# Optimization experiments

Hardware: AMD Instinct MI355X
Metric: run time of the kernel (lower is better)

The kernel has to match this reference:

```python
import jax, jax.numpy as jnp
import numpy as np

EPS = 1e-6


def _l2norm_last(x):
    return jnp.linalg.norm(x, axis=-1, keepdims=True)


def rotate_to(src, tgt):
    # rotation trick (vector-quantize-pytorch): Householder-style rotation of src onto tgt direction
    # src, tgt: (b, t, d)
    ns = _l2norm_last(src)
    nt = _l2norm_last(tgt)
    u = src / jnp.maximum(ns, EPS)
    q = tgt / jnp.maximum(nt, EPS)
    w = u + q
    w = jax.lax.stop_gradient(w / jnp.maximum(_l2norm_last(w), EPS))
    e = src
    rotated = (e
               - 2.0 * jnp.sum(e * w, axis=-1, keepdims=True) * w
               + 2.0 * jnp.sum(e * jax.lax.stop_gradient(u), axis=-1, keepdims=True) * q)
    return rotated * jax.lax.stop_gradient(nt / jnp.maximum(ns, EPS))


def _simvq_stage(res, V_i, g_i, b_i, cb_i, commit_w):
    # res: (b, t, D); V_i: (D, cd); g_i, b_i: (D,); cb_i: (cs, cd)
    # weight_norm Conv1d(k=1): W = g * V / ||V||_row
    Wn = g_i[:, None] * V_i / jnp.maximum(jnp.linalg.norm(V_i, axis=1, keepdims=True), 1e-12)
    implicit = cb_i @ Wn.T + b_i  # (cs, D) implicit codebook
    # nearest code via squared-distance argmin (cdist argmin equivalent, no_grad)
    d2 = (jnp.sum(res * res, axis=-1, keepdims=True)
          - 2.0 * jnp.einsum('btd,cd->btc', res, implicit)
          + jnp.sum(implicit * implicit, axis=-1))
    idx = jnp.argmin(d2, axis=-1)  # (b, t) int
    z_q = implicit[idx]  # gather: (b, t, D)
    commit = (jnp.mean((jax.lax.stop_gradient(res) - z_q) ** 2)
              + 0.25 * jnp.mean((res - jax.lax.stop_gradient(z_q)) ** 2))
    z_q = rotate_to(res, z_q)
    return z_q, idx, commit * commit_w


def setup_inputs() -> dict:
    key = jax.random.key(0)
    ks = jax.random.split(key, 5)
    B, D, T = 16, 512, 2048
    N, CS, CD = 9, 1024, 8
    z = jax.random.normal(ks[0], (B, D, T), dtype=jnp.float32)
    V = jax.random.normal(ks[1], (N, D, CD), dtype=jnp.float32)
    g = jax.random.uniform(ks[2], (N, D), dtype=jnp.float32, minval=0.5, maxval=1.5)
    b = jax.random.normal(ks[3], (N, D), dtype=jnp.float32) * 0.01
    CB = jax.random.normal(ks[4], (N, CS, CD), dtype=jnp.float32) * (CD ** -0.5)
    return {"z": z, "V": V, "g": g, "b": b, "CB": CB}


def reference(z, V, g, b, CB):
    # eval-mode ResidualSimVQ forward, all n_codebooks stages
    n_codebooks = V.shape[0]
    res = jnp.transpose(z, (0, 2, 1))  # (b, t, D)
    z_q = jnp.zeros_like(res)
    commitment_loss = jnp.float32(0.0)
    codes = []
    for i in range(n_codebooks):
        z_q_i, idx_i, commit_i = _simvq_stage(res, V[i], g[i], b[i], CB[i], 1.0)
        z_q = z_q + z_q_i
        res = res - z_q_i
        commitment_loss = commitment_loss + commit_i
        codes.append(idx_i)
    z_q = jnp.transpose(z_q, (0, 2, 1))  # (b, D, t)
    codes = jnp.stack(codes, axis=1)  # (b, n_codebooks, t)
    return z_q, codes, commitment_loss
```

## Files before the change

### kernel.cpp

```cpp
#include <hip/hip_runtime.h>


#define NB  16
#define DD  512
#define TT  2048
#define NCB 9
#define CS  1024
#define CD  8
#define KK  9
#define NBLK (NB * (TT / 16))
#define STGF (KK * DD * 4)
#define GAPTHR 0.015f

#define WS_WN_OFF  16384
#define WS_WNF_OFF (WS_WN_OFF  + (size_t)NCB*DD*KK*8)
#define WS_Q_OFF   (WS_WNF_OFF + (size_t)NCB*DD*KK*4)
#define WS_QF_OFF  (WS_Q_OFF   + (size_t)NCB*CS*8)

__device__ __forceinline__ void ld_lds16(const void* g, void* l) {
  __builtin_amdgcn_global_load_lds(
      (const __attribute__((address_space(1))) void*)g,
      (__attribute__((address_space(3))) void*)l, 16, 0, 0);
}

__global__ void k_wn(const float* __restrict__ V, const float* __restrict__ g,
                     const float* __restrict__ bp, double* __restrict__ wn,
                     float* __restrict__ wnf) {
  int gid = blockIdx.x * 256 + threadIdx.x;
  if (gid >= NCB * DD) return;
  int i = gid / DD, d = gid % DD;
  const float* vp = V + (size_t)gid * CD;
  double v[CD], s = 0.0;
#pragma unroll
  for (int k = 0; k < CD; k++) { v[k] = (double)vp[k]; s = fma(v[k], v[k], s); }
  double den = fmax(sqrt(s), 1e-12);
  double gg = (double)g[gid];
  double* row = wn + ((size_t)i * DD + d) * KK;
  float* fb = wnf + (size_t)i * KK * DD;
#pragma unroll
  for (int k = 0; k < CD; k++) {
    double wv = gg * v[k] / den;
    row[k] = wv;
    fb[(size_t)k * DD + d] = (float)wv;
  }
  row[CD] = (double)bp[gid];
  fb[(size_t)CD * DD + d] = bp[gid];
}

__global__ void k_q(const float* __restrict__ CBp, const float* __restrict__ bp,
                    const double* __restrict__ wn,
                    double* __restrict__ q, float* __restrict__ qf) {
  int wid = blockIdx.x * 4 + (threadIdx.x >> 6);
  int lane = threadIdx.x & 63;
  int i = wid / CS, c = wid % CS;
  const float* cb = CBp + (size_t)(i * CS + c) * CD;
  double cbv[CD];
#pragma unroll
  for (int k = 0; k < CD; k++) cbv[k] = (double)cb[k];
  const double* wnp = wn + (size_t)i * DD * KK;
  const float* bb = bp + (size_t)i * DD;
  double acc = 0.0;
#pragma unroll
  for (int j = 0; j < 8; j++) {
    int d = j * 64 + lane;
    double imp = (double)bb[d];
#pragma unroll
    for (int k = 0; k < CD; k++) imp = fma(cbv[k], wnp[(size_t)d * KK + k], imp);
    acc = fma(imp, imp, acc);
  }
#pragma unroll
  for (int o = 32; o; o >>= 1) acc += __shfl_xor(acc, o, 64);
  if (lane == 0) { q[wid] = acc; qf[wid] = (float)(0.5 * acc); }
}

__launch_bounds__(256, 2)
__global__ void k_main(const float* __restrict__ z, const float* __restrict__ CBp,
                       const double* __restrict__ wn, const float* __restrict__ wnf,
                       const double* __restrict__ qtab, const float* __restrict__ qftab,
                       float* __restrict__ out_zq, float* __restrict__ out_codes,
                       double* __restrict__ partials) {
  __shared__ __align__(16) float wbuf[2][KK * DD];
  __shared__ double cbuf[4];
  float* tile = (float*)wbuf;

  const int tid = threadIdx.x, lane = tid & 63, w = tid >> 6;
  const int bb = blockIdx.x >> 7, tg = blockIdx.x & 127;
  const int t0 = tg * 16;
  const float* zb = z + (size_t)bb * DD * TT + t0;
  const char* wfb = (const char*)wnf;

#pragma unroll
  for (int m = 0; m < 8; m++) {
    int F = tid + m * 256, d = F >> 2, qq = F & 3;
    const float4 v = *(const float4*)(zb + (size_t)d * TT + qq * 4);
    tile[d * 17 + qq * 4 + 0] = v.x; tile[d * 17 + qq * 4 + 1] = v.y;
    tile[d * 17 + qq * 4 + 2] = v.z; tile[d * 17 + qq * 4 + 3] = v.w;
  }
  __syncthreads();

  double res[4][8], ns2[4];
#pragma unroll
  for (int r = 0; r < 4; r++) {
    double s = 0.0;
#pragma unroll
    for (int j = 0; j < 8; j++) {
      res[r][j] = (double)tile[(j * 64 + lane) * 17 + (w * 4 + r)];
      s = fma(res[r][j], res[r][j], s);
    }
    ns2[r] = s;
  }
#pragma unroll
  for (int o = 32; o; o >>= 1)
#pragma unroll
    for (int r = 0; r < 4; r++) ns2[r] += __shfl_xor(ns2[r], o, 64);
  __syncthreads();

#pragma unroll
  for (int m = 0; m < 4; m++)
    ld_lds16(wfb + (w + m * 4) * 1024 + lane * 16,
             (char*)wbuf[0] + (w + m * 4) * 1024);
  if (w < 2)
    ld_lds16(wfb + (w + 16) * 1024 + lane * 16,
             (char*)wbuf[0] + (w + 16) * 1024);
  __syncthreads();

  double commit = 0.0;

  for (int i = 0; i < NCB; i++) {
    const float* wcur = wbuf[i & 1];
    if (i < NCB - 1) {
      const char* src = wfb + (size_t)(i + 1) * STGF;
      char* dst = (char*)wbuf[(i + 1) & 1];
#pragma unroll
      for (int m = 0; m < 4; m++)
        ld_lds16(src + (w + m * 4) * 1024 + lane * 16, dst + (w + m * 4) * 1024);
      if (w < 2)
        ld_lds16(src + (w + 16) * 1024 + lane * 16, dst + (w + 16) * 1024);
    }

    const float* cbbase = CBp + (size_t)i * CS * CD;
    const float* qfb = qftab + i * CS;
    const double* qb = qtab + i * CS;

    float pf[4][KK];
#pragma unroll
    for (int r = 0; r < 4; r++)
#pragma unroll
      for (int k = 0; k < KK; k++) pf[r][k] = 0.0f;
#pragma unroll
    for (int j = 0; j < 8; j++) {
      int d = j * 64 + lane;
      float wv[KK];
#pragma unroll
      for (int k = 0; k < KK; k++) wv[k] = wcur[k * DD + d];
      float rv[4];
#pragma unroll
      for (int r = 0; r < 4; r++) rv[r] = -(float)res[r][j];
#pragma unroll
      for (int r = 0; r < 4; r++)
#pragma unroll
        for (int k = 0; k < KK; k++) pf[r][k] = fmaf(rv[r], wv[k], pf[r][k]);
    }
#pragma unroll
    for (int o = 32; o; o >>= 1)
#pragma unroll
      for (int r = 0; r < 4; r++)
#pragma unroll
        for (int k = 0; k < KK; k++) pf[r][k] += __shfl_xor(pf[r][k], o, 64);

    float s1a[4], s2a[4], s1b[4], s2b[4];
    int   c1a[4], c1b[4];
#pragma unroll
    for (int r = 0; r < 4; r++) {
      s1a[r] = s2a[r] = s1b[r] = s2b[r] = 3.4e38f;
      c1a[r] = c1b[r] = 0;
    }
#pragma unroll 4
    for (int m = 0; m < 16; m += 2) {
#pragma unroll
      for (int h = 0; h < 2; h++) {
        int c = (m + h) * 64 + lane;
        const float4 c0 = *(const float4*)(cbbase + (size_t)c * CD);
        const float4 cx = *(const float4*)(cbbase + (size_t)c * CD + 4);
        float qv = qfb[c];
#pragma unroll
        for (int r = 0; r < 4; r++) {
          float s = qv;
          s = fmaf(c0.x, pf[r][0], s); s = fmaf(c0.y, pf[r][1], s);
          s = fmaf(c0.z, pf[r][2], s); s = fmaf(c0.w, pf[r][3], s);
          s = fmaf(cx.x, pf[r][4], s); s = fmaf(cx.y, pf[r][5], s);
          s = fmaf(cx.z, pf[r][6], s); s = fmaf(cx.w, pf[r][7], s);
          if (h == 0) {
            if (s < s1a[r]) { s2a[r] = s1a[r]; s1a[r] = s; c1a[r] = c; }
            else            { s2a[r] = fminf(s2a[r], s); }
          } else {
            if (s < s1b[r]) { s2b[r] = s1b[r]; s1b[r] = s; c1b[r] = c; }
            else            { s2b[r] = fminf(s2b[r], s); }
          }
        }
      }
    }
    float s1[4], s2[4]; int c1[4];
#pragma unroll
    for (int r = 0; r < 4; r++) {
      if (s1a[r] < s1b[r] || (s1a[r] == s1b[r] && c1a[r] < c1b[r])) {
        s1[r] = s1a[r]; c1[r] = c1a[r]; s2[r] = fminf(s2a[r], s1b[r]);
      } else {
        s1[r] = s1b[r]; c1[r] = c1b[r]; s2[r] = fminf(s2b[r], s1a[r]);
      }
    }
#pragma unroll
    for (int o = 32; o; o >>= 1) {
#pragma unroll
      for (int r = 0; r < 4; r++) {
        float os1 = __shfl_xor(s1[r], o, 64);
        int   oc1 = __shfl_xor(c1[r], o, 64);
        float os2 = __shfl_xor(s2[r], o, 64);
        float hi = fmaxf(s1[r], os1);
        s2[r] = fminf(fminf(s2[r], os2), hi);
        if (os1 < s1[r] || (os1 == s1[r] && oc1 < c1[r])) { s1[r] = os1; c1[r] = oc1; }
      }
    }

    double Ap[4], Cm[4];
    float cbf[4][8];
#pragma unroll
    for (int r = 0; r < 4; r++) {
      if (s2[r] - s1[r] < GAPTHR) {
        double pd[KK];
#pragma unroll
        for (int k = 0; k < KK; k++) pd[k] = 0.0;
#pragma unroll
        for (int j = 0; j < 8; j++) {
          const double* wrow = wn + ((size_t)i * DD + j * 64 + lane) * KK;
          double rv = res[r][j];
#pragma unroll
          for (int k = 0; k < KK; k++) pd[k] = fma(rv, wrow[k], pd[k]);
        }
#pragma unroll
        for (int o = 32; o; o >>= 1)
#pragma unroll
          for (int k = 0; k < KK; k++) pd[k] += __shfl_xor(pd[k], o, 64);
        double pm2[8];
#pragma unroll
        for (int k = 0; k < 8; k++) pm2[k] = -2.0 * pd[k];
        double bs = 1e300; int bc = 0;
#pragma unroll 4
        for (int m = 0; m < 16; m++) {
          int c = m * 64 + lane;
          const float* cb2 = cbbase + (size_t)c * CD;
          double s = qb[c];
#pragma unroll
          for (int k = 0; k < 8; k++) s = fma((double)cb2[k], pm2[k], s);
          if (s < bs) { bs = s; bc = c; }
        }
#pragma unroll
        for (int o = 32; o; o >>= 1) {
          double obs = __shfl_xor(bs, o, 64);
          int    obc = __shfl_xor(bc, o, 64);
          if (obs < bs || (obs == bs && obc < bc)) { bs = obs; bc = obc; }
        }
        c1[r] = bc;
      }
      int cu = __builtin_amdgcn_readfirstlane(c1[r]);
      const float* cbr = cbbase + (size_t)cu * CD;
      double pzn = (double)pf[r][8];
#pragma unroll
      for (int k = 0; k < 8; k++) {
        float cf = cbr[k];
        cbf[r][k] = cf;
        pzn = fma((double)cf, (double)pf[r][k], pzn);
      }
      double pz = -pzn;
      double nt2 = qb[cu];
      double n2 = ns2[r];
      double rns = (n2  > 1e-12) ? rsqrt(n2)  : 1e6;
      double rnt = (nt2 > 1e-12) ? rsqrt(nt2) : 1e6;
      double s_nt = nt2 * rnt;
      double wn2 = n2 * rns * rns + 2.0 * pz * rns * rnt + nt2 * rnt * rnt;
      double rdwn = (wn2 > 1e-12) ? rsqrt(wn2) : 1e6;
      double eu = n2 * rns;
      double ew = (n2 * rns + pz * rnt) * rdwn;
      double scale = s_nt * rns;
      double A = scale * (1.0 - 2.0 * ew * rdwn * rns);
      double C = scale * rnt * 2.0 * (eu - ew * rdwn);
      commit += n2 - 2.0 * pz + nt2;
      double ap = 1.0 - A;
      Ap[r] = ap; Cm[r] = C;
      ns2[r] = ap * ap * n2 - 2.0 * ap * C * pz + C * C * nt2;
      if (lane == 0)
        out_codes[((size_t)bb * NCB + i) * TT + t0 + w * 4 + r] = (float)cu;
    }

#pragma unroll
    for (int j = 0; j < 8; j++) {
      int d = j * 64 + lane;
      float wv[KK];
#pragma unroll
      for (int k = 0; k < KK; k++) wv[k] = wcur[k * DD + d];
#pragma unroll
      for (int r = 0; r < 4; r++) {
        float impf = wv[8];
#pragma unroll
        for (int k = 0; k < 8; k++) impf = fmaf(cbf[r][k], wv[k], impf);
        res[r][j] = Ap[r] * res[r][j] - Cm[r] * (double)impf;
      }
    }
    __syncthreads();
  }

  if (lane == 0) cbuf[w] = commit;

#pragma unroll
  for (int r = 0; r < 4; r++)
#pragma unroll
    for (int j = 0; j < 8; j++)
      tile[(j * 64 + lane) * 17 + (w * 4 + r)] = (float)res[r][j];
  __syncthreads();
#pragma unroll
  for (int m = 0; m < 8; m++) {
    int F = tid + m * 256, d = F >> 2, qq = F & 3;
    const float4 v = *(const float4*)(zb + (size_t)d * TT + qq * 4);
    float4 o;
    o.x = v.x - tile[d * 17 + qq * 4 + 0];
    o.y = v.y - tile[d * 17 + qq * 4 + 1];
    o.z = v.z - tile[d * 17 + qq * 4 + 2];
    o.w = v.w - tile[d * 17 + qq * 4 + 3];
    *(float4*)(out_zq + ((size_t)bb * DD + d) * TT + t0 + qq * 4) = o;
  }
  if (tid == 0)
    partials[blockIdx.x] = cbuf[0] + cbuf[1] + cbuf[2] + cbuf[3];
}

__global__ void k_fin(const double* __restrict__ partials, float* __restrict__ outc) {
  __shared__ double sb[4];
  int tid = threadIdx.x, lane = tid & 63, w = tid >> 6;
  double s = 0.0;
#pragma unroll
  for (int m = 0; m < NBLK / 256; m++) s += partials[tid + m * 256];
#pragma unroll
  for (int o = 32; o; o >>= 1) s += __shfl_xor(s, o, 64);
  if (lane == 0) sb[w] = s;
  __syncthreads();
  if (tid == 0) {
    double tot = sb[0] + sb[1] + sb[2] + sb[3];
    outc[0] = (float)(tot * 1.25 / (double)((size_t)NB * TT * DD));
  }
}

extern "C" void kernel_launch(void* const* d_in, const int* in_sizes, int n_in,
                              void* d_out, int out_size, void* d_ws, size_t ws_size,
                              hipStream_t stream) {
  const float* z  = (const float*)d_in[0];
  const float* V  = (const float*)d_in[1];
  const float* g  = (const float*)d_in[2];
  const float* b  = (const float*)d_in[3];
  const float* CB = (const float*)d_in[4];
  float* out = (float*)d_out;

  double* parts = (double*)d_ws;
  double* wn  = (double*)((char*)d_ws + WS_WN_OFF);
  float*  wnf = (float*)((char*)d_ws + WS_WNF_OFF);
  double* q   = (double*)((char*)d_ws + WS_Q_OFF);
  float*  qf  = (float*)((char*)d_ws + WS_QF_OFF);

  hipLaunchKernelGGL(k_wn, dim3((NCB * DD + 255) / 256), dim3(256), 0, stream,
                     V, g, b, wn, wnf);
  hipLaunchKernelGGL(k_q, dim3((NCB * CS) / 4), dim3(256), 0, stream, CB, b, wn, q, qf);
  hipLaunchKernelGGL(k_main, dim3(NBLK), dim3(256), 0, stream,
                     z, CB, wn, wnf, q, qf,
                     out, out + (size_t)NB * DD * TT, parts);
  hipLaunchKernelGGL(k_fin, dim3(1), dim3(256), 0, stream,
                     parts, out + (size_t)NB * DD * TT + (size_t)NB * NCB * TT);
}
```

Before: 617.8 us.

## Read per-stage weights directly from global memory in padded row layout

Removes the double-buffered LDS staging of the normalized weight matrix and instead has each thread read its weight row straight from global (L2-cached) memory, using a padded 12-float row layout that allows two float4 loads plus a scalar. This drops the per-stage barrier and the LDS footprint, so the launch bound is raised from 2 to 3 blocks per SIMD for higher occupancy. In exchange, every stage now issues global loads on the critical path of the distance and update loops, and the higher occupancy target may force register spills given the large double-precision state held per thread.

Result: slower. 796.5 us (+28.9%).

```diff
diff --git a/kernel.cpp b/kernel.cpp
--- a/kernel.cpp
+++ b/kernel.cpp
@@ -8,20 +8,14 @@
 #define CS  1024
 #define CD  8
 #define KK  9
+#define KP  12
 #define NBLK (NB * (TT / 16))
-#define STGF (KK * DD * 4)
 #define GAPTHR 0.015f
 
 #define WS_WN_OFF  16384
 #define WS_WNF_OFF (WS_WN_OFF  + (size_t)NCB*DD*KK*8)
-#define WS_Q_OFF   (WS_WNF_OFF + (size_t)NCB*DD*KK*4)
+#define WS_Q_OFF   (WS_WNF_OFF + (size_t)NCB*DD*KP*4)
 #define WS_QF_OFF  (WS_Q_OFF   + (size_t)NCB*CS*8)
-
-__device__ __forceinline__ void ld_lds16(const void* g, void* l) {
-  __builtin_amdgcn_global_load_lds(
-      (const __attribute__((address_space(1))) void*)g,
-      (__attribute__((address_space(3))) void*)l, 16, 0, 0);
-}
 
 __global__ void k_wn(const float* __restrict__ V, const float* __restrict__ g,
                      const float* __restrict__ bp, double* __restrict__ wn,
@@ -36,15 +30,16 @@
   double den = fmax(sqrt(s), 1e-12);
   double gg = (double)g[gid];
   double* row = wn + ((size_t)i * DD + d) * KK;
-  float* fb = wnf + (size_t)i * KK * DD;
+  float* frow = wnf + ((size_t)i * DD + d) * KP;
 #pragma unroll
   for (int k = 0; k < CD; k++) {
     double wv = gg * v[k] / den;
     row[k] = wv;
-    fb[(size_t)k * DD + d] = (float)wv;
+    frow[k] = (float)wv;
   }
   row[CD] = (double)bp[gid];
-  fb[(size_t)CD * DD + d] = bp[gid];
+  frow[CD] = bp[gid];
+  frow[9] = 0.0f; frow[10] = 0.0f; frow[11] = 0.0f;
 }
 
 __global__ void k_q(const float* __restrict__ CBp, const float* __restrict__ bp,
@@ -73,21 +68,19 @@
   if (lane == 0) { q[wid] = acc; qf[wid] = (float)(0.5 * acc); }
 }
 
-__launch_bounds__(256, 2)
+__launch_bounds__(256, 3)
 __global__ void k_main(const float* __restrict__ z, const float* __restrict__ CBp,
                        const double* __restrict__ wn, const float* __restrict__ wnf,
                        const double* __restrict__ qtab, const float* __restrict__ qftab,
                        float* __restrict__ out_zq, float* __restrict__ out_codes,
                        double* __restrict__ partials) {
-  __shared__ __align__(16) float wbuf[2][KK * DD];
+  __shared__ __align__(16) float tile[DD * 17];
   __shared__ double cbuf[4];
-  float* tile = (float*)wbuf;
 
   const int tid = threadIdx.x, lane = tid & 63, w = tid >> 6;
   const int bb = blockIdx.x >> 7, tg = blockIdx.x & 127;
   const int t0 = tg * 16;
   const float* zb = z + (size_t)bb * DD * TT + t0;
-  const char* wfb = (const char*)wnf;
 
 #pragma unroll
   for (int m = 0; m < 8; m++) {
@@ -113,31 +106,11 @@
   for (int o = 32; o; o >>= 1)
 #pragma unroll
     for (int r = 0; r < 4; r++) ns2[r] += __shfl_xor(ns2[r], o, 64);
-  __syncthreads();
-
-#pragma unroll
-  for (int m = 0; m < 4; m++)
-    ld_lds16(wfb + (w + m * 4) * 1024 + lane * 16,
-             (char*)wbuf[0] + (w + m * 4) * 1024);
-  if (w < 2)
-    ld_lds16(wfb + (w + 16) * 1024 + lane * 16,
-             (char*)wbuf[0] + (w + 16) * 1024);
-  __syncthreads();
 
   double commit = 0.0;
 
   for (int i = 0; i < NCB; i++) {
-    const float* wcur = wbuf[i & 1];
-    if (i < NCB - 1) {
-      const char* src = wfb + (size_t)(i + 1) * STGF;
-      char* dst = (char*)wbuf[(i + 1) & 1];
-#pragma unroll
-      for (int m = 0; m < 4; m++)
-        ld_lds16(src + (w + m * 4) * 1024 + lane * 16, dst + (w + m * 4) * 1024);
-      if (w < 2)
-        ld_lds16(src + (w + 16) * 1024 + lane * 16, dst + (w + 16) * 1024);
-    }
-
+    const float* wfp = wnf + (size_t)i * DD * KP;
     const float* cbbase = CBp + (size_t)i * CS * CD;
     const float* qfb = qftab + i * CS;
     const double* qb = qtab + i * CS;
@@ -149,17 +122,25 @@
       for (int k = 0; k < KK; k++) pf[r][k] = 0.0f;
 #pragma unroll
     for (int j = 0; j < 8; j++) {
-      int d = j * 64 + lane;
-      float wv[KK];
-#pragma unroll
-      for (int k = 0; k < KK; k++) wv[k] = wcur[k * DD + d];
+      const float* row = wfp + (size_t)(j * 64 + lane) * KP;
+      const float4 w0 = *(const float4*)(row);
+      const float4 w1 = *(const float4*)(row + 4);
+      const float  w8 = row[8];
       float rv[4];
 #pragma unroll
       for (int r = 0; r < 4; r++) rv[r] = -(float)res[r][j];
 #pragma unroll
-      for (int r = 0; r < 4; r++)
-#pragma unroll
-        for (int k = 0; k < KK; k++) pf[r][k] = fmaf(rv[r], wv[k], pf[r][k]);
+      for (int r = 0; r < 4; r++) {
+        pf[r][0] = fmaf(rv[r], w0.x, pf[r][0]);
+        pf[r][1] = fmaf(rv[r], w0.y, pf[r][1]);
+        pf[r][2] = fmaf(rv[r], w0.z, pf[r][2]);
+        pf[r][3] = fmaf(rv[r], w0.w, pf[r][3]);
+        pf[r][4] = fmaf(rv[r], w1.x, pf[r][4]);
+        pf[r][5] = fmaf(rv[r], w1.y, pf[r][5]);
+        pf[r][6] = fmaf(rv[r], w1.z, pf[r][6]);
+        pf[r][7] = fmaf(rv[r], w1.w, pf[r][7]);
+        pf[r][8] = fmaf(rv[r], w8,   pf[r][8]);
+      }
     }
 #pragma unroll
     for (int o = 32; o; o >>= 1)
@@ -294,23 +275,29 @@
 
 #pragma unroll
     for (int j = 0; j < 8; j++) {
-      int d = j * 64 + lane;
-      float wv[KK];
-#pragma unroll
-      for (int k = 0; k < KK; k++) wv[k] = wcur[k * DD + d];
+      const float* row = wfp + (size_t)(j * 64 + lane) * KP;
+      const float4 w0 = *(const float4*)(row);
+      const float4 w1 = *(const float4*)(row + 4);
+      const float  w8 = row[8];
 #pragma unroll
       for (int r = 0; r < 4; r++) {
-        float impf = wv[8];
-#pragma unroll
-        for (int k = 0; k < 8; k++) impf = fmaf(cbf[r][k], wv[k], impf);
+        float impf = w8;
+        impf = fmaf(cbf[r][0], w0.x, impf);
+        impf = fmaf(cbf[r][1], w0.y, impf);
+        impf = fmaf(cbf[r][2], w0.z, impf);
+        impf = fmaf(cbf[r][3], w0.w, impf);
+        impf = fmaf(cbf[r][4], w1.x, impf);
+        impf = fmaf(cbf[r][5], w1.y, impf);
+        impf = fmaf(cbf[r][6], w1.z, impf);
+        impf = fmaf(cbf[r][7], w1.w, impf);
         res[r][j] = Ap[r] * res[r][j] - Cm[r] * (double)impf;
       }
     }
-    __syncthreads();
   }
 
   if (lane == 0) cbuf[w] = commit;
 
+  __syncthreads();
 #pragma unroll
   for (int r = 0; r < 4; r++)
 #pragma unroll
```
